# Kernel tuning notes

Measured on AMD Instinct MI355X. Metric: run time of the kernel, lower is better.

The kernel has to match this reference:

```python
import jax, jax.numpy as jnp
import numpy as np

RC = 4.6  # cutoff radius (Angstrom), from init_kwargs
FACTOR = 7.199822675975224  # constants.half_Hartree * constants.Bohr (eV*A)


def exp_cutoff(d, rc):
    # smooth exponential (bump) cutoff: exp(1 - 1/(1-(d/rc)^2)) for d<rc, else 0
    x = d / rc
    inside = x < 1.0
    xs = jnp.where(inside, x, 0.5)  # safe value to avoid nan in masked branch
    f = jnp.exp(1.0 - 1.0 / (1.0 - xs * xs))
    return jnp.where(inside, f, 0.0)


def setup_inputs() -> dict:
    key = jax.random.key(0)
    k1, k2 = jax.random.split(key)
    B, N = 64, 512
    # atoms in a 40 A box -> realistic long-range distances
    coord = jax.random.uniform(k1, (B, N, 3), dtype=jnp.float32) * 40.0
    charges = jax.random.normal(k2, (B, N), dtype=jnp.float32) * 0.3
    mask = jnp.ones((B, N), dtype=bool)  # all atoms valid (no padding)
    return {"coord": coord, "charges": charges, "mask": mask}


def reference(coord, charges, mask):
    # coul_simple: e = factor * sum_ij (1 - fc(d_ij)) * q_i * q_j / d_ij, per molecule
    B, N, _ = coord.shape
    pair_mask = mask[:, :, None] & mask[:, None, :]
    eye = jnp.eye(N, dtype=bool)[None]
    valid = pair_mask & ~eye  # mask self-pairs and padding (mask_ij_)
    disp = coord[:, :, None, :] - coord[:, None, :, :]          # [B,N,N,3]
    d2 = jnp.sum(disp * disp, axis=-1)                          # [B,N,N]
    d = jnp.sqrt(jnp.where(valid, d2, 1.0))                     # safe sqrt on diag
    fc = 1.0 - exp_cutoff(d, RC)
    qq = charges[:, :, None] * charges[:, None, :]              # q_i * q_j
    e_ij = jnp.where(valid, fc * qq / d, 0.0)
    return FACTOR * jnp.sum(e_ij, axis=(1, 2))                  # mol_sum -> [B]
```

## Files before the change

### kernel.cpp

```cpp
#include <hip/hip_runtime.h>

#define N_ATOMS 512
#define SPLITS  16
#define IPB     (N_ATOMS / SPLITS)
#define BLOCK   256
#define JSTRIDE (BLOCK / IPB)

__global__ __launch_bounds__(BLOCK) void coul_kernel(
    const float* __restrict__ coord,
    const float* __restrict__ charges,
    float* __restrict__ out)
{
    const int b = blockIdx.x / SPLITS;
    const int s = blockIdx.x % SPLITS;

    __shared__ float sx[N_ATOMS], sy[N_ATOMS], sz[N_ATOMS], sq[N_ATOMS];

    const float* c = coord   + (size_t)b * N_ATOMS * 3;
    const float* q = charges + (size_t)b * N_ATOMS;

    for (int k = threadIdx.x; k < N_ATOMS; k += BLOCK) {
        sx[k] = c[3 * k + 0];
        sy[k] = c[3 * k + 1];
        sz[k] = c[3 * k + 2];
        sq[k] = q[k];
    }
    __syncthreads();

    const int t  = threadIdx.x;
    const int i  = s * IPB + (t / JSTRIDE);
    const int j0 = t % JSTRIDE;

    const float xi = sx[i], yi = sy[i], zi = sz[i], qi = sq[i];
    const float inv_rc2 = 1.0f / (4.6f * 4.6f);

    float acc = 0.0f;
    for (int j = j0; j < N_ATOMS; j += JSTRIDE) {
        if (j == i) continue;
        float dx = xi - sx[j];
        float dy = yi - sy[j];
        float dz = zi - sz[j];
        float d2 = dx * dx + dy * dy + dz * dz;
        float rinv = rsqrtf(d2);
        float term = qi * sq[j] * rinv;
        float x2 = d2 * inv_rc2;
        if (x2 < 1.0f) {
            term *= (1.0f - __expf(1.0f - 1.0f / (1.0f - x2)) * 0.0f
                          - expf(1.0f - 1.0f / (1.0f - x2)));
        }
        acc += term;
    }

    #pragma unroll
    for (int off = 32; off > 0; off >>= 1)
        acc += __shfl_down(acc, off, 64);

    __shared__ float wsum[BLOCK / 64];
    if ((t & 63) == 0) wsum[t >> 6] = acc;
    __syncthreads();

    if (t == 0) {
        float blk = wsum[0] + wsum[1] + wsum[2] + wsum[3];
        atomicAdd(&out[b], 7.199822675975224f * blk);
    }
}

extern "C" void kernel_launch(void* const* d_in, const int* in_sizes, int n_in,
                              void* d_out, int out_size, void* d_ws, size_t ws_size,
                              hipStream_t stream) {
    const float* coord   = (const float*)d_in[0];
    const float* charges = (const float*)d_in[1];
    float* out = (float*)d_out;

    const int B = in_sizes[1] / N_ATOMS;

    hipMemsetAsync(d_out, 0, (size_t)out_size * sizeof(float), stream);

    coul_kernel<<<B * SPLITS, BLOCK, 0, stream>>>(coord, charges, out);
}
```

Baseline: 75.76 us.

## Exploit pair symmetry to halve pair evaluations and pack atoms as float4

Uses the i-j symmetry of the pair energy: each atom now visits only the next half of the atoms in cyclic order (256 partners), with the antipodal pair weighted by one half, and the final sum is doubled. Atom data is packed into a single float4 shared array so each partner needs one LDS load, and the dead __expf term is removed. The memset-plus-atomicAdd accumulation is replaced by per-block partials in the workspace and a small second reduce kernel. This roughly halves the arithmetic but adds a second kernel launch and depends on the hard-coded N=512 and split count.

Result: faster. 65.90 us (-13.0%).

```diff
diff --git a/kernel.cpp b/kernel.cpp
--- a/kernel.cpp
+++ b/kernel.cpp
@@ -2,53 +2,56 @@
 
 #define N_ATOMS 512
 #define SPLITS  16
-#define IPB     (N_ATOMS / SPLITS)
+#define IPB     32
 #define BLOCK   256
-#define JSTRIDE (BLOCK / IPB)
+#define JSTR    8
 
-__global__ __launch_bounds__(BLOCK) void coul_kernel(
+__global__ __launch_bounds__(BLOCK) void coul_pair_kernel(
     const float* __restrict__ coord,
     const float* __restrict__ charges,
-    float* __restrict__ out)
+    float* __restrict__ partials)
 {
-    const int b = blockIdx.x / SPLITS;
-    const int s = blockIdx.x % SPLITS;
+    const int b = blockIdx.x >> 4;
+    const int s = blockIdx.x & 15;
 
-    __shared__ float sx[N_ATOMS], sy[N_ATOMS], sz[N_ATOMS], sq[N_ATOMS];
+    __shared__ float4 atom[N_ATOMS];
 
     const float* c = coord   + (size_t)b * N_ATOMS * 3;
     const float* q = charges + (size_t)b * N_ATOMS;
-
-    for (int k = threadIdx.x; k < N_ATOMS; k += BLOCK) {
-        sx[k] = c[3 * k + 0];
-        sy[k] = c[3 * k + 1];
-        sz[k] = c[3 * k + 2];
-        sq[k] = q[k];
-    }
+    for (int k = threadIdx.x; k < N_ATOMS; k += BLOCK)
+        atom[k] = make_float4(c[3 * k], c[3 * k + 1], c[3 * k + 2], q[k]);
     __syncthreads();
 
     const int t  = threadIdx.x;
-    const int i  = s * IPB + (t / JSTRIDE);
-    const int j0 = t % JSTRIDE;
+    const int j0 = t & (JSTR - 1);
+    const int i  = s * IPB + (t >> 3);
 
-    const float xi = sx[i], yi = sy[i], zi = sz[i], qi = sq[i];
+    const float4 ai = atom[i];
     const float inv_rc2 = 1.0f / (4.6f * 4.6f);
 
     float acc = 0.0f;
-    for (int j = j0; j < N_ATOMS; j += JSTRIDE) {
-        if (j == i) continue;
-        float dx = xi - sx[j];
-        float dy = yi - sy[j];
-        float dz = zi - sz[j];
+    int j = (i + 1 + j0) & (N_ATOMS - 1);
+    #pragma unroll 4
+    for (int k = 0; k < 31; ++k) {
+        const float4 aj = atom[j];
+        j = (j + JSTR) & (N_ATOMS - 1);
+        float dx = ai.x - aj.x, dy = ai.y - aj.y, dz = ai.z - aj.z;
         float d2 = dx * dx + dy * dy + dz * dz;
-        float rinv = rsqrtf(d2);
-        float term = qi * sq[j] * rinv;
+        float term = ai.w * aj.w * rsqrtf(d2);
         float x2 = d2 * inv_rc2;
-        if (x2 < 1.0f) {
-            term *= (1.0f - __expf(1.0f - 1.0f / (1.0f - x2)) * 0.0f
-                          - expf(1.0f - 1.0f / (1.0f - x2)));
-        }
+        if (x2 < 1.0f)
+            term *= (1.0f - expf(1.0f - 1.0f / (1.0f - x2)));
         acc += term;
+    }
+    {
+        const float4 aj = atom[j];
+        float dx = ai.x - aj.x, dy = ai.y - aj.y, dz = ai.z - aj.z;
+        float d2 = dx * dx + dy * dy + dz * dz;
+        float term = ai.w * aj.w * rsqrtf(d2);
+        float x2 = d2 * inv_rc2;
+        if (x2 < 1.0f)
+            term *= (1.0f - expf(1.0f - 1.0f / (1.0f - x2)));
+        acc += (j0 == JSTR - 1) ? 0.5f * term : term;
     }
 
     #pragma unroll
@@ -58,10 +61,19 @@
     __shared__ float wsum[BLOCK / 64];
     if ((t & 63) == 0) wsum[t >> 6] = acc;
     __syncthreads();
+    if (t == 0)
+        partials[blockIdx.x] = wsum[0] + wsum[1] + wsum[2] + wsum[3];
+}
 
-    if (t == 0) {
-        float blk = wsum[0] + wsum[1] + wsum[2] + wsum[3];
-        atomicAdd(&out[b], 7.199822675975224f * blk);
+__global__ void coul_reduce_kernel(const float* __restrict__ partials,
+                                   float* __restrict__ out, int B)
+{
+    const int b = threadIdx.x;
+    if (b < B) {
+        float sum = 0.0f;
+        #pragma unroll
+        for (int s = 0; s < SPLITS; ++s) sum += partials[b * SPLITS + s];
+        out[b] = 2.0f * 7.199822675975224f * sum;
     }
 }
 
@@ -70,11 +82,11 @@
                               hipStream_t stream) {
     const float* coord   = (const float*)d_in[0];
     const float* charges = (const float*)d_in[1];
-    float* out = (float*)d_out;
+    float* out      = (float*)d_out;
+    float* partials = (float*)d_ws;
 
     const int B = in_sizes[1] / N_ATOMS;
 
-    hipMemsetAsync(d_out, 0, (size_t)out_size * sizeof(float), stream);
-
-    coul_kernel<<<B * SPLITS, BLOCK, 0, stream>>>(coord, charges, out);
+    coul_pair_kernel<<<B * SPLITS, BLOCK, 0, stream>>>(coord, charges, partials);
+    coul_reduce_kernel<<<1, 64, 0, stream>>>(partials, out, B);
 }
```
